# Performance work log

Hardware: AMD Instinct MI355X
Metric: run time of the kernel (lower is better)

## Reference

```python
import jax, jax.numpy as jnp
import numpy as np

N = 4_194_304  # total observations
NBAND = 8      # photometric bands


def setup_inputs() -> dict:
    key = jax.random.key(0)
    ks = jax.random.split(key, 6)
    t = jnp.sort(jax.random.uniform(ks[0], (N,), dtype=jnp.float32) * 10000.0)
    band = jax.random.randint(ks[1], (N,), 0, NBAND)
    y = jax.random.normal(ks[2], (N,), dtype=jnp.float32) * 0.5
    diag = jax.random.uniform(ks[3], (N,), dtype=jnp.float32) * 0.1 + 0.01
    log_amp_delta = jax.random.normal(ks[4], (NBAND - 1,), dtype=jnp.float32) * 0.1
    lag = jax.random.uniform(ks[5], (NBAND - 1,), dtype=jnp.float32) * 5.0
    # exponential (DRW) celerite term: k(tau) = a * exp(-c * tau)
    log_kernel_param = jnp.array([0.0, -3.0], dtype=jnp.float32)
    return {"t": t, "band": band, "y": y, "diag": diag,
            "log_amp_delta": log_amp_delta, "lag": lag,
            "log_kernel_param": log_kernel_param}


def reference(t, band, y, diag, log_amp_delta, lag, log_kernel_param):
    # amp/lag transforms: prepend 0 for the reference band (jnp.insert at 0)
    log_amps = jnp.concatenate([jnp.zeros((1,), log_amp_delta.dtype), log_amp_delta])
    lags = jnp.concatenate([jnp.zeros((1,), lag.dtype), lag])

    # lag-shift times per band, then sort (GP requires sorted inputs)
    new_t = t - lags[band]
    inds = jnp.argsort(new_t)
    ts, bs, ys, ds = new_t[inds], band[inds], y[inds], diag[inds]

    # multiband kernel: K_ij = amp_i * amp_j * a * exp(-c * |t_i - t_j|) + diag_i * delta_ij
    amps = jnp.exp(log_amps)[bs]                 # [N]
    a = jnp.exp(log_kernel_param[0])
    c = jnp.exp(log_kernel_param[1])
    A = ds + a * amps * amps                     # diagonal of K
    U = a * amps                                 # low-rank left factor
    V = amps                                     # low-rank right factor
    dt = jnp.diff(ts, prepend=ts[:1])            # dt[0] = 0
    phi = jnp.exp(-c * dt)                       # transfer factor between neighbors

    # celerite O(N) Cholesky + forward solve (single real term -> scalar state)
    def step(carry, xs):
        Sp, fp = carry                           # Sp = S_{n-1} + D W^2, fp = f_{n-1} + W z
        A_n, U_n, V_n, phi_n, r_n = xs
        S = phi_n * phi_n * Sp
        D = A_n - U_n * U_n * S
        W = (V_n - U_n * S) / D
        f = phi_n * fp
        z = r_n - U_n * f
        return (S + D * W * W, f + W * z), (D, z)

    init = (jnp.zeros((), ys.dtype), jnp.zeros((), ys.dtype))
    _, (D, z) = jax.lax.scan(step, init, (A, U, V, phi, ys))

    n = ys.shape[0]
    log2pi = jnp.log(2 * jnp.pi).astype(ys.dtype)
    logp = -0.5 * (jnp.sum(z * z / D) + jnp.sum(jnp.log(D)) + n * log2pi)
    return -logp  # LCModel.__call__ returns negative log-probability
```

## Files before the change

kernel.cpp:

```cpp
#include <hip/hip_runtime.h>
#include <hip/hip_bf16.h>
#include <hip/hip_fp16.h>
#include <math.h>

#define NBAND 8
#define K1_THREADS 1024
#define CHUNK 128
#define HALO  128
#define TILE  16
#define OUTBLK 2048
#define MCAP   2432
#define SEG    32
#define NSEG   128
#define NPART  512

struct Params {
  float lags[NBAND];
  float amps[NBAND];
  float inv_amp[NBAND];
  float inv_amp2[NBAND];
  float a, c, kphi1, kphi2;
  int bandstart[NBAND];
  int nb[NBAND];
  int blkbase[NBAND + 1];
};

__device__ __forceinline__ unsigned f2u(float f) {
  unsigned b = __float_as_uint(f);
  return b ^ ((b >> 31) ? 0xFFFFFFFFu : 0x80000000u);
}
__device__ __forceinline__ float u2f(unsigned u) {
  unsigned m = (u & 0x80000000u) ? 0x80000000u : 0xFFFFFFFFu;
  return __uint_as_float(u ^ m);
}

__global__ void k1_hist(const int* __restrict__ band, int* __restrict__ cnt) {
  __shared__ int wc[16][NBAND];
  int tid = threadIdx.x;
  int i = blockIdx.x * K1_THREADS + tid;
  int b = band[i];
  int lane = tid & 63, w = tid >> 6;
#pragma unroll
  for (int bb = 0; bb < NBAND; ++bb) {
    unsigned long long m = __ballot(b == bb);
    if (lane == bb) wc[w][bb] = __popcll(m);
  }
  __syncthreads();
  if (tid < NBAND) {
    int s = 0;
#pragma unroll
    for (int w2 = 0; w2 < 16; ++w2) s += wc[w2][tid];
    cnt[blockIdx.x * NBAND + tid] = s;
  }
}

__global__ void k2a_segsum(const int* __restrict__ cnt, int* __restrict__ segsum) {
  int s = blockIdx.x * 256 + threadIdx.x;
  if (s >= NSEG * NBAND) return;
  int b = s & 7, seg = s >> 3;
  int base = seg * SEG;
  int sum = 0;
#pragma unroll 8
  for (int u = 0; u < SEG; ++u) sum += cnt[(base + u) * NBAND + b];
  segsum[s] = sum;
}

__global__ void k2b_scan(const int* __restrict__ segsum, int* __restrict__ segbase,
                         Params* __restrict__ P,
                         const float* __restrict__ lad, const float* __restrict__ lag,
                         const float* __restrict__ lkp) {
  __shared__ int sd[NSEG * NBAND];
  __shared__ int tot[NBAND], bstart[NBAND];
  int tid = threadIdx.x;
  if (tid == 0) {
    P->lags[0] = 0.f;
    P->amps[0] = 1.f;
    P->inv_amp[0] = 1.f;
    P->inv_amp2[0] = 1.f;
    for (int j = 0; j < NBAND - 1; ++j) {
      P->lags[j + 1] = lag[j];
      float am = expf(lad[j]);
      P->amps[j + 1] = am;
      float ia = expf(-lad[j]);
      P->inv_amp[j + 1] = ia;
      P->inv_amp2[j + 1] = ia * ia;
    }
    float a = expf(lkp[0]);
    float c = expf(lkp[1]);
    P->a = a;
    P->c = c;
    P->kphi1 = -c * 1.4426950408889634f;
    P->kphi2 = -2.f * c * 1.4426950408889634f;
  }
  int b = tid & 7, seg = tid >> 3;
  int sum = segsum[tid];
  int val = sum;
  sd[tid] = val;
  __syncthreads();
  for (int off = 1; off < NSEG; off <<= 1) {
    int yv = (seg >= off) ? sd[tid - off * NBAND] : 0;
    __syncthreads();
    val += yv;
    sd[tid] = val;
    __syncthreads();
  }
  if (seg == NSEG - 1) tot[b] = val;
  __syncthreads();
  if (tid == 0) {
    int g = 0;
    for (int bb = 0; bb < NBAND; ++bb) {
      bstart[bb] = g;
      P->bandstart[bb] = g;
      P->nb[bb] = tot[bb];
      g += tot[bb];
    }
    int s = 0;
    for (int bb = 0; bb < NBAND; ++bb) {
      P->blkbase[bb] = s;
      s += (tot[bb] + 255) / 256;
    }
    P->blkbase[NBAND] = s;
  }
  __syncthreads();
  segbase[tid] = bstart[b] + (val - sum);
}

__global__ void k2c_boff(const int* __restrict__ cnt, const int* __restrict__ segbase,
                         int* __restrict__ boff) {
  int s = blockIdx.x * 256 + threadIdx.x;
  if (s >= NSEG * NBAND) return;
  int b = s & 7, seg = s >> 3;
  int base = seg * SEG;
  int run = segbase[s];
  for (int u = 0; u < SEG; ++u) {
    int idx = (base + u) * NBAND + b;
    int x = cnt[idx];
    boff[idx] = run;
    run += x;
  }
}

__global__ void k3_scatter(const float* __restrict__ t, const int* __restrict__ band,
                           const float* __restrict__ y, const float* __restrict__ dg,
                           const int* __restrict__ boff, const Params* __restrict__ P,
                           unsigned* __restrict__ pay2, float* __restrict__ bt) {
  __shared__ int wc[16][NBAND];
  int tid = threadIdx.x;
  int i = blockIdx.x * K1_THREADS + tid;
  int b = band[i];
  float v = t[i] - P->lags[b];
  int lane = tid & 63, w = tid >> 6;
  int lower = 0;
#pragma unroll
  for (int bb = 0; bb < NBAND; ++bb) {
    unsigned long long m = __ballot(b == bb);
    if (lane == bb) wc[w][bb] = __popcll(m);
    if (b == bb) lower = __popcll(m & ((1ull << lane) - 1ull));
  }
  __syncthreads();
  int base = 0;
  for (int w2 = 0; w2 < w; ++w2) base += wc[w2][b];
  int pos = boff[blockIdx.x * NBAND + b] + base + lower;
  float yp = y[i] * P->inv_amp[b];
  float dp = dg[i] * P->inv_amp2[b];
  unsigned yx = __float_as_uint(yp);
  unsigned yb = (yx + 0x7FFFu + ((yx >> 16) & 1u)) >> 16;
  unsigned db = (unsigned)__half_as_ushort(__float2half(dp));
  pay2[pos] = (yb << 16) | db;
  bt[pos] = v;
}

__global__ void k4a_cuts(const float* __restrict__ bt, const Params* __restrict__ P,
                         int* __restrict__ cuts, int nout) {
  int s = blockIdx.x * 64 + threadIdx.x;
  if (s >= (nout + 1) * NBAND) return;
  int oo = s >> 3, b = s & 7;
  int res;
  if (oo == 0) res = 0;
  else if (oo == nout) res = P->nb[b];
  else {
    float vmin = bt[P->bandstart[0]];
    float vmax = bt[P->bandstart[0] + P->nb[0] - 1];
#pragma unroll
    for (int bb = 1; bb < NBAND; ++bb) {
      vmin = fminf(vmin, bt[P->bandstart[bb]]);
      vmax = fmaxf(vmax, bt[P->bandstart[bb] + P->nb[bb] - 1]);
    }
    float v = vmin + (float)((double)(vmax - vmin) * oo / nout);
    unsigned svu = f2u(v);
    const float* p = bt + P->bandstart[b];
    int lo = 0, hi = P->nb[b];
    while (lo < hi) {
      int mid = (lo + hi) >> 1;
      if (f2u(p[mid]) < svu) lo = mid + 1; else hi = mid;
    }
    res = lo;
  }
  cuts[oo * NBAND + b] = res;
}

__global__ __launch_bounds__(256) void k4_merge(const float* __restrict__ bt,
                                                const unsigned* __restrict__ pay2,
                                                const Params* __restrict__ P,
                                                const int* __restrict__ cuts,
                                                float2* __restrict__ out8) {
  __shared__ unsigned long long bufA[MCAP];
  __shared__ unsigned long long bufB[MCAP];
  __shared__ int klo[NBAND], offs[NBAND + 1];
  __shared__ int sbs[NBAND];
  __shared__ long R0s;
  int tid = threadIdx.x;
  int o = blockIdx.x;
  if (tid < NBAND) sbs[tid] = P->bandstart[tid];
  if (tid == 0) {
    int s = 0;
    long r0 = 0;
    for (int b = 0; b < NBAND; ++b) {
      int lo = cuts[o * NBAND + b];
      int hi = cuts[(o + 1) * NBAND + b];
      klo[b] = lo;
      offs[b] = s;
      s += hi - lo;
      r0 += lo;
    }
    offs[NBAND] = s;
    R0s = r0;
  }
  __syncthreads();
  int M = offs[NBAND];
  if (M > MCAP) return;
  int ro[NBAND + 1];
#pragma unroll
  for (int b = 0; b <= NBAND; ++b) ro[b] = offs[b];
  for (int p = tid; p < M; p += 256) {
    int b = 0;
#pragma unroll
    for (int bb = 1; bb < NBAND; ++bb) b += (p >= ro[bb]);
    int w = p - ro[b];
    unsigned u = f2u(bt[sbs[b] + klo[b] + w]);
    bufA[p] = ((unsigned long long)u << 15) | ((unsigned long long)b << 12) | (unsigned)w;
  }
  __syncthreads();
#pragma unroll
  for (int r = 0; r < 3; ++r) {
    const unsigned long long* src = (r == 1) ? bufB : bufA;
    unsigned long long* dst = (r == 1) ? bufA : bufB;
    int h = 1 << r;
    int tpm = 64 << r;
    int mi = tid / tpm, tt = tid % tpm;
    int g = mi * 2 * h;
    int a1 = offs[g], a2 = offs[g + h], a3 = offs[g + 2 * h];
    int n1 = a2 - a1, n2 = a3 - a2;
    int total = n1 + n2;
    int e0 = (int)((long)tt * total / tpm);
    int e1 = (int)((long)(tt + 1) * total / tpm);
    int lo = max(0, e0 - n2), hi = min(e0, n1);
    while (lo < hi) {
      int mid = (lo + hi) >> 1;
      if (src[a1 + mid] < src[a2 + (e0 - mid) - 1]) lo = mid + 1; else hi = mid;
    }
    int i = lo, j = e0 - lo;
    unsigned long long x = (i < n1) ? src[a1 + i] : ~0ull;
    unsigned long long yv = (j < n2) ? src[a2 + j] : ~0ull;
    for (int k = e0; k < e1; ++k) {
      bool tk = x < yv;
      dst[a1 + k] = tk ? x : yv;
      if (tk) { ++i; x = (i < n1) ? src[a1 + i] : ~0ull; }
      else    { ++j; yv = (j < n2) ? src[a2 + j] : ~0ull; }
    }
    __syncthreads();
  }
  long R0 = R0s;
  for (int p = tid; p < M; p += 256) {
    unsigned long long rec = bufB[p];
    int b = (int)((rec >> 12) & 7);
    int w = (int)(rec & 0xFFF);
    unsigned key = (unsigned)(rec >> 15);
    unsigned pv = pay2[sbs[b] + klo[b] + w];
    out8[R0 + p] = make_float2(u2f(key), __uint_as_float(pv));
  }
}

struct ScanState {
  float Sp, fp, tprev, s1, s2;
};

template <bool ACCUM>
__device__ __forceinline__ void step_one(float2 v, ScanState& st, float a, float a2,
                                         float k1c, float k2c) {
  float t = v.x;
  unsigned pv = __float_as_uint(v.y);
  float yv = __uint_as_float(pv & 0xFFFF0000u);
  float d = __half2float(__ushort_as_half((unsigned short)(pv & 0xFFFFu)));
  float dt = t - st.tprev;
  st.tprev = t;
  float e2 = __builtin_amdgcn_exp2f(k2c * dt);
  float e1 = __builtin_amdgcn_exp2f(k1c * dt);
  float Aa = d + a;
  float c1 = d - a;
  float x = e2 * st.Sp;
  float D = fmaf(-a2, x, Aa);
  float r = __builtin_amdgcn_rcpf(D);
  float num = fmaf(c1, x, 1.0f);
  st.Sp = num * r;
  float f = e1 * st.fp;
  float z = fmaf(-a, f, yv);
  float Wn = fmaf(-a, x, 1.0f);
  float W = Wn * r;
  st.fp = fmaf(W, z, f);
  if (ACCUM) {
    st.s1 = fmaf(z * z, r, st.s1);
    st.s2 += __builtin_amdgcn_logf(D);
  }
}

template <bool ACCUM>
__device__ __forceinline__ void run_range(const float2* __restrict__ q, long s, long e,
                                          ScanState& st, float a, float a2, float k1c,
                                          float k2c) {
  float2 A[TILE], B[TILE];
#pragma unroll
  for (int u = 0; u < TILE; ++u) A[u] = q[s + u];
  for (long tb = s; tb < e; tb += 2 * TILE) {
#pragma unroll
    for (int u = 0; u < TILE; ++u) B[u] = q[tb + TILE + u];
#pragma unroll
    for (int u = 0; u < TILE; ++u) step_one<ACCUM>(A[u], st, a, a2, k1c, k2c);
#pragma unroll
    for (int u = 0; u < TILE; ++u) A[u] = q[tb + 2 * TILE + u];
#pragma unroll
    for (int u = 0; u < TILE; ++u) step_one<ACCUM>(B[u], st, a, a2, k1c, k2c);
  }
}

__global__ __launch_bounds__(64, 1) void k5_scan(const float2* __restrict__ q,
                                                 const Params* __restrict__ P,
                                                 double2* __restrict__ part) {
  int k = blockIdx.x * 64 + threadIdx.x;
  long base = (long)k * CHUNK;
  float a = P->a, a2 = a * a, k1c = P->kphi1, k2c = P->kphi2;
  ScanState st;
  st.Sp = 0.f;
  st.fp = 0.f;
  st.s1 = 0.f;
  st.s2 = 0.f;
  long s0 = (k == 0) ? base : (base - HALO);
  st.tprev = q[s0].x;
  if (k > 0) run_range<false>(q, base - HALO, base, st, a, a2, k1c, k2c);
  run_range<true>(q, base, base + CHUNK, st, a, a2, k1c, k2c);
  float s1 = st.s1, s2 = st.s2;
#pragma unroll
  for (int off = 32; off > 0; off >>= 1) {
    s1 += __shfl_down(s1, off);
    s2 += __shfl_down(s2, off);
  }
  if (threadIdx.x == 0) part[blockIdx.x] = make_double2((double)s1, (double)s2);
}

__global__ void k6_final(const double2* __restrict__ part, const Params* __restrict__ P,
                         const float* __restrict__ lad, float* __restrict__ out, long n) {
  int tid = threadIdx.x;
  double s1 = 0.0, s2 = 0.0;
  for (int u = tid; u < NPART; u += 64) {
    double2 p = part[u];
    s1 += p.x;
    s2 += p.y;
  }
#pragma unroll
  for (int off = 32; off > 0; off >>= 1) {
    s1 += __shfl_down(s1, off);
    s2 += __shfl_down(s2, off);
  }
  if (tid == 0) {
    double ampc = 0.0;
    for (int b = 1; b < NBAND; ++b) ampc += (double)P->nb[b] * (double)lad[b - 1];
    double r = 0.5 * (s1 + s2 * 0.6931471805599453 + (double)n * 1.8378770664093453)
               + ampc;
    out[0] = (float)r;
  }
}

extern "C" void kernel_launch(void* const* d_in, const int* in_sizes, int n_in,
                              void* d_out, int out_size, void* d_ws, size_t ws_size,
                              hipStream_t stream) {
  const float* t = (const float*)d_in[0];
  const int* band = (const int*)d_in[1];
  const float* y = (const float*)d_in[2];
  const float* dg = (const float*)d_in[3];
  const float* lad = (const float*)d_in[4];
  const float* lag = (const float*)d_in[5];
  const float* lkp = (const float*)d_in[6];
  float* out = (float*)d_out;
  long N = in_sizes[0];

  char* ws = (char*)d_ws;
  Params* P = (Params*)(ws + 0);
  double2* part = (double2*)(ws + 4096);
  int* cnt = (int*)(ws + 16384);
  long nblk = N / K1_THREADS;
  int* boff = (int*)(ws + 147456);
  int* segsum = (int*)(ws + 278528);
  int* segbase = (int*)(ws + 282624);
  int nout = (int)(N / OUTBLK);
  int* cuts = (int*)(ws + 294912);
  float2* out8 = (float2*)(ws + 524288);
  unsigned* pay2 = (unsigned*)(ws + 524288 + (size_t)N * 8);
  float* bt = (float*)(ws + 524288 + (size_t)N * 12);

  k1_hist<<<(int)nblk, K1_THREADS, 0, stream>>>(band, cnt);
  k2a_segsum<<<(NSEG * NBAND + 255) / 256, 256, 0, stream>>>(cnt, segsum);
  k2b_scan<<<1, NSEG * NBAND, 0, stream>>>(segsum, segbase, P, lad, lag, lkp);
  k2c_boff<<<(NSEG * NBAND + 255) / 256, 256, 0, stream>>>(cnt, segbase, boff);
  k3_scatter<<<(int)nblk, K1_THREADS, 0, stream>>>(t, band, y, dg, boff, P, pay2, bt);
  int ncut = ((nout + 1) * NBAND + 63) / 64;
  k4a_cuts<<<ncut, 64, 0, stream>>>(bt, P, cuts, nout);
  k4_merge<<<nout, 256, 0, stream>>>(bt, pay2, P, cuts, out8);
  long T = N / CHUNK;
  k5_scan<<<(int)(T / 64), 64, 0, stream>>>(out8, P, part);
  k6_final<<<1, 64, 0, stream>>>(part, P, lad, out, N);
}
```

Baseline: 201.3 us.

## Fuse prefix-scan stages and pack time key with payload into single record

Folds the segment-sum into the histogram kernel via atomics and replaces the boff kernel with an in-block prefix over up to 31 counts in the scatter kernel. The cuts kernel is also folded into the merge blocks. The scatter now writes one 64-bit record holding the order-preserving time key and the packed payload, so the merge loads records directly and writes the output without a second gather of the payload. This removes three kernel launches and one random gather, at the cost of redundant cut searches per block and a memset.

```diff
diff --git a/kernel.cpp b/kernel.cpp
--- a/kernel.cpp
+++ b/kernel.cpp
@@ -16,13 +16,11 @@
 
 struct Params {
   float lags[NBAND];
-  float amps[NBAND];
   float inv_amp[NBAND];
   float inv_amp2[NBAND];
   float a, c, kphi1, kphi2;
   int bandstart[NBAND];
   int nb[NBAND];
-  int blkbase[NBAND + 1];
 };
 
 __device__ __forceinline__ unsigned f2u(float f) {
@@ -34,7 +32,8 @@
   return __uint_as_float(u ^ m);
 }
 
-__global__ void k1_hist(const int* __restrict__ band, int* __restrict__ cnt) {
+__global__ void k1_hist(const int* __restrict__ band, int* __restrict__ cnt,
+                        int* __restrict__ segsum) {
   __shared__ int wc[16][NBAND];
   int tid = threadIdx.x;
   int i = blockIdx.x * K1_THREADS + tid;
@@ -51,18 +50,8 @@
 #pragma unroll
     for (int w2 = 0; w2 < 16; ++w2) s += wc[w2][tid];
     cnt[blockIdx.x * NBAND + tid] = s;
-  }
-}
-
-__global__ void k2a_segsum(const int* __restrict__ cnt, int* __restrict__ segsum) {
-  int s = blockIdx.x * 256 + threadIdx.x;
-  if (s >= NSEG * NBAND) return;
-  int b = s & 7, seg = s >> 3;
-  int base = seg * SEG;
-  int sum = 0;
-#pragma unroll 8
-  for (int u = 0; u < SEG; ++u) sum += cnt[(base + u) * NBAND + b];
-  segsum[s] = sum;
+    atomicAdd(&segsum[(blockIdx.x >> 5) * NBAND + tid], s);
+  }
 }
 
 __global__ void k2b_scan(const int* __restrict__ segsum, int* __restrict__ segbase,
@@ -74,13 +63,10 @@
   int tid = threadIdx.x;
   if (tid == 0) {
     P->lags[0] = 0.f;
-    P->amps[0] = 1.f;
     P->inv_amp[0] = 1.f;
     P->inv_amp2[0] = 1.f;
     for (int j = 0; j < NBAND - 1; ++j) {
       P->lags[j + 1] = lag[j];
-      float am = expf(lad[j]);
-      P->amps[j + 1] = am;
       float ia = expf(-lad[j]);
       P->inv_amp[j + 1] = ia;
       P->inv_amp2[j + 1] = ia * ia;
@@ -114,39 +100,21 @@
       P->nb[bb] = tot[bb];
       g += tot[bb];
     }
-    int s = 0;
-    for (int bb = 0; bb < NBAND; ++bb) {
-      P->blkbase[bb] = s;
-      s += (tot[bb] + 255) / 256;
-    }
-    P->blkbase[NBAND] = s;
   }
   __syncthreads();
   segbase[tid] = bstart[b] + (val - sum);
-}
-
-__global__ void k2c_boff(const int* __restrict__ cnt, const int* __restrict__ segbase,
-                         int* __restrict__ boff) {
-  int s = blockIdx.x * 256 + threadIdx.x;
-  if (s >= NSEG * NBAND) return;
-  int b = s & 7, seg = s >> 3;
-  int base = seg * SEG;
-  int run = segbase[s];
-  for (int u = 0; u < SEG; ++u) {
-    int idx = (base + u) * NBAND + b;
-    int x = cnt[idx];
-    boff[idx] = run;
-    run += x;
-  }
 }
 
 __global__ void k3_scatter(const float* __restrict__ t, const int* __restrict__ band,
                            const float* __restrict__ y, const float* __restrict__ dg,
-                           const int* __restrict__ boff, const Params* __restrict__ P,
-                           unsigned* __restrict__ pay2, float* __restrict__ bt) {
+                           const int* __restrict__ cnt, const int* __restrict__ segbase,
+                           const Params* __restrict__ P,
+                           unsigned long long* __restrict__ rec8) {
   __shared__ int wc[16][NBAND];
-  int tid = threadIdx.x;
-  int i = blockIdx.x * K1_THREADS + tid;
+  __shared__ int sboff[NBAND];
+  int tid = threadIdx.x;
+  int bid = blockIdx.x;
+  int i = bid * K1_THREADS + tid;
   int b = band[i];
   float v = t[i] - P->lags[b];
   int lane = tid & 63, w = tid >> 6;
@@ -157,71 +125,73 @@
     if (lane == bb) wc[w][bb] = __popcll(m);
     if (b == bb) lower = __popcll(m & ((1ull << lane) - 1ull));
   }
-  __syncthreads();
-  int base = 0;
-  for (int w2 = 0; w2 < w; ++w2) base += wc[w2][b];
-  int pos = boff[blockIdx.x * NBAND + b] + base + lower;
+  if (tid < NBAND) {
+    int seg = bid >> 5, r = bid & 31;
+    int s = segbase[seg * NBAND + tid];
+    int base = seg * SEG;
+    for (int u = 0; u < r; ++u) s += cnt[(base + u) * NBAND + tid];
+    sboff[tid] = s;
+  }
+  __syncthreads();
+  int base2 = 0;
+  for (int w2 = 0; w2 < w; ++w2) base2 += wc[w2][b];
+  int pos = sboff[b] + base2 + lower;
   float yp = y[i] * P->inv_amp[b];
   float dp = dg[i] * P->inv_amp2[b];
   unsigned yx = __float_as_uint(yp);
   unsigned yb = (yx + 0x7FFFu + ((yx >> 16) & 1u)) >> 16;
   unsigned db = (unsigned)__half_as_ushort(__float2half(dp));
-  pay2[pos] = (yb << 16) | db;
-  bt[pos] = v;
-}
-
-__global__ void k4a_cuts(const float* __restrict__ bt, const Params* __restrict__ P,
-                         int* __restrict__ cuts, int nout) {
-  int s = blockIdx.x * 64 + threadIdx.x;
-  if (s >= (nout + 1) * NBAND) return;
-  int oo = s >> 3, b = s & 7;
-  int res;
-  if (oo == 0) res = 0;
-  else if (oo == nout) res = P->nb[b];
-  else {
-    float vmin = bt[P->bandstart[0]];
-    float vmax = bt[P->bandstart[0] + P->nb[0] - 1];
-#pragma unroll
-    for (int bb = 1; bb < NBAND; ++bb) {
-      vmin = fminf(vmin, bt[P->bandstart[bb]]);
-      vmax = fmaxf(vmax, bt[P->bandstart[bb] + P->nb[bb] - 1]);
-    }
-    float v = vmin + (float)((double)(vmax - vmin) * oo / nout);
-    unsigned svu = f2u(v);
-    const float* p = bt + P->bandstart[b];
-    int lo = 0, hi = P->nb[b];
-    while (lo < hi) {
-      int mid = (lo + hi) >> 1;
-      if (f2u(p[mid]) < svu) lo = mid + 1; else hi = mid;
-    }
-    res = lo;
-  }
-  cuts[oo * NBAND + b] = res;
-}
-
-__global__ __launch_bounds__(256) void k4_merge(const float* __restrict__ bt,
-                                                const unsigned* __restrict__ pay2,
+  unsigned pay = (yb << 16) | db;
+  rec8[pos] = ((unsigned long long)f2u(v) << 32) | pay;
+}
+
+__global__ __launch_bounds__(256) void k4_merge(const unsigned long long* __restrict__ rec8,
                                                 const Params* __restrict__ P,
-                                                const int* __restrict__ cuts,
-                                                float2* __restrict__ out8) {
+                                                float2* __restrict__ out8, int nout) {
   __shared__ unsigned long long bufA[MCAP];
   __shared__ unsigned long long bufB[MCAP];
+  __shared__ int cut2[2][NBAND];
   __shared__ int klo[NBAND], offs[NBAND + 1];
   __shared__ int sbs[NBAND];
   __shared__ long R0s;
   int tid = threadIdx.x;
   int o = blockIdx.x;
   if (tid < NBAND) sbs[tid] = P->bandstart[tid];
+  if (tid < 16) {
+    int b = tid & 7, which = tid >> 3;
+    int oo = o + which;
+    int res;
+    if (oo == 0) res = 0;
+    else if (oo >= nout) res = P->nb[b];
+    else {
+      float vmin = u2f((unsigned)(rec8[P->bandstart[0]] >> 32));
+      float vmax = u2f((unsigned)(rec8[P->bandstart[0] + P->nb[0] - 1] >> 32));
+#pragma unroll
+      for (int bb = 1; bb < NBAND; ++bb) {
+        vmin = fminf(vmin, u2f((unsigned)(rec8[P->bandstart[bb]] >> 32)));
+        vmax = fmaxf(vmax, u2f((unsigned)(rec8[P->bandstart[bb] + P->nb[bb] - 1] >> 32)));
+      }
+      float v = vmin + (float)((double)(vmax - vmin) * oo / nout);
+      unsigned svu = f2u(v);
+      const unsigned long long* p = rec8 + P->bandstart[b];
+      int lo = 0, hi = P->nb[b];
+      while (lo < hi) {
+        int mid = (lo + hi) >> 1;
+        if ((unsigned)(p[mid] >> 32) < svu) lo = mid + 1; else hi = mid;
+      }
+      res = lo;
+    }
+    cut2[which][b] = res;
+  }
+  __syncthreads();
   if (tid == 0) {
     int s = 0;
     long r0 = 0;
     for (int b = 0; b < NBAND; ++b) {
-      int lo = cuts[o * NBAND + b];
-      int hi = cuts[(o + 1) * NBAND + b];
-      klo[b] = lo;
+      klo[b] = cut2[0][b];
       offs[b] = s;
-      s += hi - lo;
-      r0 += lo;
+      s += cut2[1][b] - cut2[0][b];
+      r0 += cut2[0][b];
     }
     offs[NBAND] = s;
     R0s = r0;
@@ -237,8 +207,7 @@
 #pragma unroll
     for (int bb = 1; bb < NBAND; ++bb) b += (p >= ro[bb]);
     int w = p - ro[b];
-    unsigned u = f2u(bt[sbs[b] + klo[b] + w]);
-    bufA[p] = ((unsigned long long)u << 15) | ((unsigned long long)b << 12) | (unsigned)w;
+    bufA[p] = rec8[sbs[b] + klo[b] + w];
   }
   __syncthreads();
 #pragma unroll
@@ -273,11 +242,8 @@
   long R0 = R0s;
   for (int p = tid; p < M; p += 256) {
     unsigned long long rec = bufB[p];
-    int b = (int)((rec >> 12) & 7);
-    int w = (int)(rec & 0xFFF);
-    unsigned key = (unsigned)(rec >> 15);
-    unsigned pv = pay2[sbs[b] + klo[b] + w];
-    out8[R0 + p] = make_float2(u2f(key), __uint_as_float(pv));
+    out8[R0 + p] = make_float2(u2f((unsigned)(rec >> 32)),
+                               __uint_as_float((unsigned)rec));
   }
 }
 
@@ -396,25 +362,19 @@
   char* ws = (char*)d_ws;
   Params* P = (Params*)(ws + 0);
   double2* part = (double2*)(ws + 4096);
-  int* cnt = (int*)(ws + 16384);
+  int* segsum = (int*)(ws + 16384);
+  int* segbase = (int*)(ws + 20480);
+  int* cnt = (int*)(ws + 24576);
   long nblk = N / K1_THREADS;
-  int* boff = (int*)(ws + 147456);
-  int* segsum = (int*)(ws + 278528);
-  int* segbase = (int*)(ws + 282624);
   int nout = (int)(N / OUTBLK);
-  int* cuts = (int*)(ws + 294912);
   float2* out8 = (float2*)(ws + 524288);
-  unsigned* pay2 = (unsigned*)(ws + 524288 + (size_t)N * 8);
-  float* bt = (float*)(ws + 524288 + (size_t)N * 12);
-
-  k1_hist<<<(int)nblk, K1_THREADS, 0, stream>>>(band, cnt);
-  k2a_segsum<<<(NSEG * NBAND + 255) / 256, 256, 0, stream>>>(cnt, segsum);
+  unsigned long long* rec8 = (unsigned long long*)(ws + 524288 + (size_t)N * 8);
+
+  hipMemsetAsync(segsum, 0, 4096, stream);
+  k1_hist<<<(int)nblk, K1_THREADS, 0, stream>>>(band, cnt, segsum);
   k2b_scan<<<1, NSEG * NBAND, 0, stream>>>(segsum, segbase, P, lad, lag, lkp);
-  k2c_boff<<<(NSEG * NBAND + 255) / 256, 256, 0, stream>>>(cnt, segbase, boff);
-  k3_scatter<<<(int)nblk, K1_THREADS, 0, stream>>>(t, band, y, dg, boff, P, pay2, bt);
-  int ncut = ((nout + 1) * NBAND + 63) / 64;
-  k4a_cuts<<<ncut, 64, 0, stream>>>(bt, P, cuts, nout);
-  k4_merge<<<nout, 256, 0, stream>>>(bt, pay2, P, cuts, out8);
+  k3_scatter<<<(int)nblk, K1_THREADS, 0, stream>>>(t, band, y, dg, cnt, segbase, P, rec8);
+  k4_merge<<<nout, 256, 0, stream>>>(rec8, P, out8, nout);
   long T = N / CHUNK;
   k5_scan<<<(int)(T / 64), 64, 0, stream>>>(out8, P, part);
   k6_final<<<1, 64, 0, stream>>>(part, P, lad, out, N);
```

Result: slower. 216.1 us (+7.4%).
